# Kernel tuning notes

Measured on AMD Instinct MI355X. Metric: run time of the kernel, lower is better.

Reference implementation:

```python
import jax, jax.numpy as jnp
import numpy as np

B, ES, D, A, E, H, V, T = 8, 14, 2048, 700, 700, 700, 30000, 31


def setup_inputs() -> dict:
    key = jax.random.key(0)
    ks = jax.random.split(key, 16)
    def rn(k, shape, s=0.02):
        return jax.random.normal(k, shape, jnp.float32) * s
    return {
        "encoder_out": jax.random.normal(ks[0], (B, ES, ES, D), jnp.float32),
        "encoded_captions": jax.random.randint(ks[1], (B, T), 0, V),
        "emb": jax.random.uniform(ks[2], (V, E), jnp.float32, -0.1, 0.1),
        "W_enc_att": rn(ks[3], (D, A)), "b_enc_att": jnp.zeros((A,), jnp.float32),
        "W_dec_att": rn(ks[4], (H, A)), "b_dec_att": jnp.zeros((A,), jnp.float32),
        "W_full": rn(ks[5], (A, 1)), "b_full": jnp.zeros((1,), jnp.float32),
        "W_ih": rn(ks[6], (E + D, 4 * H)), "b_ih": jnp.zeros((4 * H,), jnp.float32),
        "W_hh": rn(ks[7], (H, 4 * H)), "b_hh": jnp.zeros((4 * H,), jnp.float32),
        "W_init_h": rn(ks[8], (D, H)), "b_init_h": jnp.zeros((H,), jnp.float32),
        "W_init_c": rn(ks[9], (D, H)), "b_init_c": jnp.zeros((H,), jnp.float32),
        "W_fbeta": rn(ks[10], (H, D)), "b_fbeta": jnp.zeros((D,), jnp.float32),
        "W_fc": jax.random.uniform(ks[11], (H, V), jnp.float32, -0.1, 0.1),
        "b_fc": jnp.zeros((V,), jnp.float32),
    }


def reference(encoder_out, encoded_captions, emb,
              W_enc_att, b_enc_att, W_dec_att, b_dec_att, W_full, b_full,
              W_ih, b_ih, W_hh, b_hh, W_init_h, b_init_h, W_init_c, b_init_c,
              W_fbeta, b_fbeta, W_fc, b_fc):
    # teacher=False path: greedy decode with argmax feedback. Dropout in eval mode (identity).
    Bn = encoder_out.shape[0]
    Dd = encoder_out.shape[-1]
    enc = encoder_out.reshape(Bn, -1, Dd)          # (B, P, D)
    decode_length = encoded_captions.shape[1] - 1
    mean_enc = enc.mean(axis=1)
    h0 = mean_enc @ W_init_h + b_init_h            # (B, H)
    c0 = mean_enc @ W_init_c + b_init_c
    att1 = enc @ W_enc_att + b_enc_att             # (B, P, A) — hoisted out of the loop (same math)
    prev0 = jnp.ones((Bn,), jnp.int32)             # preds initialized to ones

    def step(carry, _):
        h, c, prev = carry
        x_emb = emb[prev]                                          # (B, E)
        att2 = h @ W_dec_att + b_dec_att                           # (B, A)
        e = (jax.nn.relu(att1 + att2[:, None, :]) @ W_full)[..., 0] + b_full[0]  # (B, P)
        alpha = jax.nn.softmax(e, axis=1)
        awe = jnp.einsum('bp,bpd->bd', alpha, enc)                 # attention-weighted encoding
        gate = jax.nn.sigmoid(h @ W_fbeta + b_fbeta)
        awe = gate * awe
        x = jnp.concatenate([x_emb, awe], axis=1)                  # (B, E+D)
        gates = x @ W_ih + b_ih + h @ W_hh + b_hh                  # (B, 4H), torch gate order i,f,g,o
        i, f, g, o = jnp.split(gates, 4, axis=1)
        c_new = jax.nn.sigmoid(f) * c + jax.nn.sigmoid(i) * jnp.tanh(g)
        h_new = jax.nn.sigmoid(o) * jnp.tanh(c_new)
        logits = h_new @ W_fc + b_fc                               # (B, V)
        prev_new = jnp.argmax(logits, axis=1).astype(jnp.int32)
        return (h_new, c_new, prev_new), (logits, alpha)

    _, (logits_seq, alpha_seq) = jax.lax.scan(step, (h0, c0, prev0), None, length=decode_length)
    predictions = jnp.transpose(logits_seq, (1, 0, 2))             # (B, T-1, V)
    alphas = jnp.transpose(alpha_seq, (1, 0, 2))                   # (B, T-1, P)
    return predictions, alphas
```

## Files before the change

### kernel.cpp

```cpp
#include <hip/hip_runtime.h>
#include <math.h>

#define BQ 8
#define PP 196
#define DD 2048
#define AA 700
#define HH 700
#define EE 700
#define VV 30000
#define NSTEP 30
#define G4 2800
#define NA 2748
#define KD 3448

#define KSA 32
#define KRA 22
#define NCBA 11

#define KSD 32
#define KRD 108
#define NCBD 11

#define KSE 6
#define KRE 117
#define NCBE 118
#define NB2 235

__device__ __forceinline__ float sigm(float x) { return 1.f / (1.f + expf(-x)); }

__global__ __launch_bounds__(256) void k_mean(const float* __restrict__ enc,
                                              float* __restrict__ mean) {
    int b = blockIdx.x >> 3;
    int d = ((blockIdx.x & 7) << 8) + threadIdx.x;
    const float* p = enc + (size_t)b * PP * DD + d;
    float s = 0.f;
    for (int i = 0; i < PP; i++) s += p[(size_t)i * DD];
    mean[b * DD + d] = s * (1.0f / PP);
}

__global__ __launch_bounds__(256) void k_init_hc(const float* __restrict__ mean,
    const float* __restrict__ Wh, const float* __restrict__ bh,
    const float* __restrict__ Wc, const float* __restrict__ bc,
    float* __restrict__ h, float* __restrict__ c) {
    __shared__ float X[BQ][DD];
    __shared__ float red[4][64][BQ];
    int tid = threadIdx.x;
    for (int i = tid; i < BQ * DD; i += 256) X[i / DD][i % DD] = mean[i];
    __syncthreads();
    int j = blockIdx.x * 64 + (tid & 63);
    int kq = tid >> 6;
    float acc[BQ];
    #pragma unroll
    for (int b = 0; b < BQ; b++) acc[b] = 0.f;
    if (j < 2 * HH) {
        bool isH = j < HH;
        int col = isH ? j : j - HH;
        const float* wp = (isH ? Wh : Wc) + (size_t)(kq * 512) * HH + col;
        for (int k = kq * 512; k < kq * 512 + 512; k++) {
            float wv = *wp; wp += HH;
            #pragma unroll
            for (int b = 0; b < BQ; b++) acc[b] += X[b][k] * wv;
        }
    }
    #pragma unroll
    for (int b = 0; b < BQ; b++) red[kq][tid & 63][b] = acc[b];
    __syncthreads();
    for (int idx = tid; idx < 512; idx += 256) {
        int jj = idx >> 3, b = idx & 7;
        int jg = blockIdx.x * 64 + jj;
        if (jg >= 2 * HH) continue;
        float s = red[0][jj][b] + red[1][jj][b] + red[2][jj][b] + red[3][jj][b];
        bool isH = jg < HH;
        int col = isH ? jg : jg - HH;
        s += isH ? bh[col] : bc[col];
        (isH ? h : c)[b * HH + col] = s;
    }
}

__global__ __launch_bounds__(256) void k_att1(const float* __restrict__ Aenc,
    const float* __restrict__ W, float* __restrict__ out0,
    float* __restrict__ out1) {
    const int M = BQ * PP;
    __shared__ float As[16][68];
    __shared__ float Bs[16][68];
    int bm = blockIdx.x, bn = blockIdx.y, bz = blockIdx.z;
    int tid = threadIdx.x;
    int tx = tid & 15, ty = tid >> 4;
    float acc[4][4] = {};
    int kbeg = bz * 1024, kend = kbeg + 1024;
    for (int kt = kbeg; kt < kend; kt += 16) {
        {
            int row = tid >> 2, k4 = (tid & 3) * 4;
            int grow = bm * 64 + row;
            float4 v = make_float4(0.f, 0.f, 0.f, 0.f);
            if (grow < M) v = *(const float4*)&Aenc[(size_t)grow * DD + kt + k4];
            As[k4 + 0][row] = v.x; As[k4 + 1][row] = v.y;
            As[k4 + 2][row] = v.z; As[k4 + 3][row] = v.w;
        }
        {
            int rk = tid >> 4, n4 = (tid & 15) * 4;
            int col = bn * 64 + n4;
            float4 wv = make_float4(0.f, 0.f, 0.f, 0.f);
            if (col < AA) wv = *(const float4*)&W[(size_t)(kt + rk) * AA + col];
            *(float4*)&Bs[rk][n4] = wv;
        }
        __syncthreads();
        #pragma unroll
        for (int k = 0; k < 16; k++) {
            float4 a  = *(const float4*)&As[k][ty * 4];
            float4 bv = *(const float4*)&Bs[k][tx * 4];
            float av[4] = {a.x, a.y, a.z, a.w};
            float bb[4] = {bv.x, bv.y, bv.z, bv.w};
            #pragma unroll
            for (int i = 0; i < 4; i++)
                #pragma unroll
                for (int j = 0; j < 4; j++) acc[i][j] += av[i] * bb[j];
        }
        __syncthreads();
    }
    float* out = bz ? out1 : out0;
    for (int i = 0; i < 4; i++) {
        int row = bm * 64 + ty * 4 + i;
        if (row >= M) continue;
        for (int j = 0; j < 4; j++) {
            int col = bn * 64 + tx * 4 + j;
            if (col < AA) out[(size_t)row * AA + col] = acc[i][j];
        }
    }
}

__global__ __launch_bounds__(256) void k_att1red(float* __restrict__ att1,
    const float* __restrict__ part, const float* __restrict__ bias) {
    size_t row = blockIdx.x;
    for (int c = threadIdx.x; c < AA; c += 256)
        att1[row * AA + c] += part[row * AA + c] + bias[c];
}

__global__ __launch_bounds__(256) void k_stepA(const float* __restrict__ h,
    const float* __restrict__ Wda, const float* __restrict__ Wfb,
    float* __restrict__ pA,
    const float* __restrict__ argval, const int* __restrict__ argidx,
    int* __restrict__ prev, int t) {
    int tid = threadIdx.x;
    if (blockIdx.x == NCBA * KSA) {
        int b = tid >> 5, l = tid & 31;
        if (b < 8) {
            if (t == 0) {
                if (l == 0) prev[b] = 1;
            } else {
                float bv = -3.4e38f; int bi = 0x7fffffff;
                for (int vb = l; vb < NB2; vb += 32) {
                    float v = argval[vb * 8 + b]; int ix = argidx[vb * 8 + b];
                    if (v > bv || (v == bv && ix < bi)) { bv = v; bi = ix; }
                }
                #pragma unroll
                for (int off = 16; off; off >>= 1) {
                    float ov = __shfl_down(bv, off, 32);
                    int   oi = __shfl_down(bi, off, 32);
                    if (ov > bv || (ov == bv && oi < bi)) { bv = ov; bi = oi; }
                }
                if (l == 0) prev[b] = bi;
            }
        }
        return;
    }
    __shared__ float s_X[KRA * 8];
    __shared__ float s_red[4 * 64 * 33];
    int cb = blockIdx.x % NCBA, kc = blockIdx.x / NCBA;
    int k0 = kc * KRA;
    int kr = min(KRA, AA - k0);
    for (int i = tid; i < kr * 8; i += 256) {
        int k = i >> 3, b = i & 7;
        s_X[k * 8 + b] = h[b * HH + k0 + k];
    }
    __syncthreads();
    int lane = tid & 63, w = tid >> 6;
    int ka = (w * kr) >> 2, kb = ((w + 1) * kr) >> 2;
    int c0 = cb * 256 + lane * 4;
    float acc[8][4] = {};
    if (c0 < NA) {
        const float* W; int col, ld;
        if (c0 < AA) { W = Wda; col = c0;      ld = AA; }
        else         { W = Wfb; col = c0 - AA; ld = DD; }
        const float* wp = W + (size_t)(k0 + ka) * ld + col;
        #pragma unroll 2
        for (int k = ka; k < kb; ++k) {
            float4 wv = *(const float4*)wp; wp += ld;
            float4 xa = *(const float4*)&s_X[k * 8];
            float4 xb = *(const float4*)&s_X[k * 8 + 4];
            float xv[8] = {xa.x, xa.y, xa.z, xa.w, xb.x, xb.y, xb.z, xb.w};
            #pragma unroll
            for (int b = 0; b < 8; b++) {
                acc[b][0] += xv[b] * wv.x; acc[b][1] += xv[b] * wv.y;
                acc[b][2] += xv[b] * wv.z; acc[b][3] += xv[b] * wv.w;
            }
        }
    }
    float* rr = &s_red[(w * 64 + lane) * 33];
    #pragma unroll
    for (int b = 0; b < 8; b++)
        #pragma unroll
        for (int cc = 0; cc < 4; cc++) rr[cc * 8 + b] = acc[b][cc];
    __syncthreads();
    for (int idx = tid; idx < 2048; idx += 256) {
        int b = idx >> 8, cl = idx & 255;
        int gc = cb * 256 + cl;
        if (gc < NA) {
            int ln = cl >> 2, cc = cl & 3;
            float s = s_red[(0 * 64 + ln) * 33 + cc * 8 + b]
                    + s_red[(1 * 64 + ln) * 33 + cc * 8 + b]
                    + s_red[(2 * 64 + ln) * 33 + cc * 8 + b]
                    + s_red[(3 * 64 + ln) * 33 + cc * 8 + b];
            pA[((size_t)kc * 8 + b) * NA + gc] = s;
        }
    }
}

__global__ __launch_bounds__(256) void k_stepB(const float* __restrict__ pA,
    const float* __restrict__ bda, const float* __restrict__ att1,
    const float* __restrict__ Wf, float* __restrict__ ebuf) {
    int b  = blockIdx.x / 49;
    int p0 = (blockIdx.x % 49) * 4;
    __shared__ float a2[AA];
    __shared__ float wf[AA];
    int tid = threadIdx.x, lane = tid & 63, w = tid >> 6;
    for (int i = tid; i < AA; i += 256) {
        float s = bda[i];
        #pragma unroll 8
        for (int kc = 0; kc < KSA; kc++) s += pA[((size_t)kc * 8 + b) * NA + i];
        a2[i] = s;
        wf[i] = Wf[i];
    }
    __syncthreads();
    int p = p0 + w;
    const float* ap = att1 + (size_t)(b * PP + p) * AA;
    float s = 0.f;
    for (int f4 = lane; f4 < 175; f4 += 64) {
        float4 av = *(const float4*)(ap + f4 * 4);
        float4 tv = *(const float4*)&a2[f4 * 4];
        float4 wv = *(const float4*)&wf[f4 * 4];
        s += fmaxf(av.x + tv.x, 0.f) * wv.x + fmaxf(av.y + tv.y, 0.f) * wv.y
           + fmaxf(av.z + tv.z, 0.f) * wv.z + fmaxf(av.w + tv.w, 0.f) * wv.w;
    }
    #pragma unroll
    for (int off = 32; off; off >>= 1) s += __shfl_down(s, off, 64);
    if (lane == 0) ebuf[b * PP + p] = s;
}

__global__ __launch_bounds__(256) void k_stepC(const float* __restrict__ enc,
    const float* __restrict__ pA, const float* __restrict__ bfb,
    const float* __restrict__ ebuf, float* __restrict__ awe,
    float* __restrict__ oalpha, int t) {
    int b = blockIdx.x >> 3, dc = blockIdx.x & 7;
    __shared__ float s_al[PP];
    __shared__ float s_gate[256];
    __shared__ float s_red[4][256];
    __shared__ float s_rb[8];
    int tid = threadIdx.x, lane = tid & 63, w = tid >> 6;
    float v = (tid < PP) ? ebuf[b * PP + tid] : -3.4e38f;
    float m = v;
    #pragma unroll
    for (int off = 32; off; off >>= 1) m = fmaxf(m, __shfl_down(m, off, 64));
    if (lane == 0) s_rb[w] = m;
    __syncthreads();
    m = fmaxf(fmaxf(s_rb[0], s_rb[1]), fmaxf(s_rb[2], s_rb[3]));
    float ex = (tid < PP) ? expf(v - m) : 0.f;
    float s2 = ex;
    #pragma unroll
    for (int off = 32; off; off >>= 1) s2 += __shfl_down(s2, off, 64);
    if (lane == 0) s_rb[4 + w] = s2;
    __syncthreads();
    float den = s_rb[4] + s_rb[5] + s_rb[6] + s_rb[7];
    if (tid < PP) {
        float al = ex / den;
        s_al[tid] = al;
        if (dc == 0) oalpha[((size_t)b * NSTEP + t) * PP + tid] = al;
    }
    {
        int d = dc * 256 + tid;
        float g = bfb[d];
        #pragma unroll 8
        for (int kc = 0; kc < KSA; kc++) g += pA[((size_t)kc * 8 + b) * NA + AA + d];
        s_gate[tid] = sigm(g);
    }
    __syncthreads();
    int d4 = dc * 256 + lane * 4;
    const float* ep = enc + ((size_t)b * PP + w * 49) * DD + d4;
    float4 acc = make_float4(0.f, 0.f, 0.f, 0.f);
    #pragma unroll 7
    for (int p = 0; p < 49; ++p) {
        float a = s_al[w * 49 + p];
        float4 ev = *(const float4*)ep; ep += DD;
        acc.x += a * ev.x; acc.y += a * ev.y;
        acc.z += a * ev.z; acc.w += a * ev.w;
    }
    *(float4*)&s_red[w][lane * 4] = acc;
    __syncthreads();
    float tot = s_red[0][tid] + s_red[1][tid] + s_red[2][tid] + s_red[3][tid];
    awe[b * DD + dc * 256 + tid] = s_gate[tid] * tot;
}

__global__ __launch_bounds__(256) void k_stepD1(const float* __restrict__ emb,
    const float* __restrict__ awe, const float* __restrict__ h,
    const float* __restrict__ Wih, const float* __restrict__ Whh,
    const int* __restrict__ prev, float* __restrict__ pD) {
    __shared__ float s_X[KRD * 8];
    __shared__ float s_red[4 * 64 * 33];
    __shared__ int s_prev[8];
    int tid = threadIdx.x;
    int cb = blockIdx.x % NCBD, kc = blockIdx.x / NCBD;
    int k0 = kc * KRD;
    int kr = min(KRD, KD - k0);
    if (tid < 8) s_prev[tid] = prev[tid];
    __syncthreads();
    for (int i = tid; i < kr * 8; i += 256) {
        int k = i >> 3, b = i & 7;
        int kg = k0 + k;
        float x;
        if (kg < EE)            x = emb[(size_t)s_prev[b] * EE + kg];
        else if (kg < EE + DD)  x = awe[b * DD + (kg - EE)];
        else                    x = h[b * HH + (kg - EE - DD)];
        s_X[k * 8 + b] = x;
    }
    __syncthreads();
    int lane = tid & 63, w = tid >> 6;
    int ka = (w * kr) >> 2, kb2 = ((w + 1) * kr) >> 2;
    int c0 = cb * 256 + lane * 4;
    float acc[8][4] = {};
    if (c0 < G4) {
        #pragma unroll 2
        for (int k = ka; k < kb2; ++k) {
            int kg = k0 + k;
            const float* wp = (kg < EE + DD)
                ? (Wih + (size_t)kg * G4 + c0)
                : (Whh + (size_t)(kg - EE - DD) * G4 + c0);
            float4 wv = *(const float4*)wp;
            float4 xa = *(const float4*)&s_X[k * 8];
            float4 xb = *(const float4*)&s_X[k * 8 + 4];
            float xv[8] = {xa.x, xa.y, xa.z, xa.w, xb.x, xb.y, xb.z, xb.w};
            #pragma unroll
            for (int b = 0; b < 8; b++) {
                acc[b][0] += xv[b] * wv.x; acc[b][1] += xv[b] * wv.y;
                acc[b][2] += xv[b] * wv.z; acc[b][3] += xv[b] * wv.w;
            }
        }
    }
    float* rr = &s_red[(w * 64 + lane) * 33];
    #pragma unroll
    for (int b = 0; b < 8; b++)
        #pragma unroll
        for (int cc = 0; cc < 4; cc++) rr[cc * 8 + b] = acc[b][cc];
    __syncthreads();
    for (int idx = tid; idx < 2048; idx += 256) {
        int b = idx >> 8, cl = idx & 255;
        int gc = cb * 256 + cl;
        if (gc < G4) {
            int ln = cl >> 2, cc = cl & 3;
            float s = s_red[(0 * 64 + ln) * 33 + cc * 8 + b]
                    + s_red[(1 * 64 + ln) * 33 + cc * 8 + b]
                    + s_red[(2 * 64 + ln) * 33 + cc * 8 + b]
                    + s_red[(3 * 64 + ln) * 33 + cc * 8 + b];
            pD[((size_t)kc * 8 + b) * G4 + gc] = s;
        }
    }
}

__global__ __launch_bounds__(256) void k_stepD2(const float* __restrict__ pD,
    const float* __restrict__ bih, const float* __restrict__ bhh,
    float* __restrict__ c, float* __restrict__ h) {
    __shared__ float sd[4][64][4];
    int tid = threadIdx.x;
    int p = tid & 63, kcg = tid >> 6;
    int oid = blockIdx.x * 64 + p;
    float g0 = 0.f, g1 = 0.f, g2 = 0.f, g3 = 0.f;
    if (oid < BQ * HH) {
        int b = oid / HH, j = oid % HH;
        #pragma unroll
        for (int u = 0; u < 8; ++u) {
            const float* base = pD + ((size_t)(kcg * 8 + u) * 8 + b) * G4;
            g0 += base[j];          g1 += base[HH + j];
            g2 += base[2 * HH + j]; g3 += base[3 * HH + j];
        }
    }
    sd[kcg][p][0] = g0; sd[kcg][p][1] = g1;
    sd[kcg][p][2] = g2; sd[kcg][p][3] = g3;
    __syncthreads();
    if (tid < 64) {
        int oid2 = blockIdx.x * 64 + tid;
        if (oid2 < BQ * HH) {
            int b = oid2 / HH, j = oid2 % HH;
            float s0 = sd[0][tid][0] + sd[1][tid][0] + sd[2][tid][0] + sd[3][tid][0]
                     + bih[j] + bhh[j];
            float s1 = sd[0][tid][1] + sd[1][tid][1] + sd[2][tid][1] + sd[3][tid][1]
                     + bih[HH + j] + bhh[HH + j];
            float s2 = sd[0][tid][2] + sd[1][tid][2] + sd[2][tid][2] + sd[3][tid][2]
                     + bih[2 * HH + j] + bhh[2 * HH + j];
            float s3 = sd[0][tid][3] + sd[1][tid][3] + sd[2][tid][3] + sd[3][tid][3]
                     + bih[3 * HH + j] + bhh[3 * HH + j];
            float ig = sigm(s0), fg = sigm(s1), gg = tanhf(s2), og = sigm(s3);
            float cn = fg * c[b * HH + j] + ig * gg;
            c[b * HH + j] = cn;
            h[b * HH + j] = og * tanhf(cn);
        }
    }
}

__global__ __launch_bounds__(256) void k_stepE1(const float* __restrict__ h,
    const float* __restrict__ Wfc, float* __restrict__ pE) {
    __shared__ float s_X[KRE * 8];
    __shared__ float s_red[4 * 64 * 33];
    int tid = threadIdx.x;
    int cb = blockIdx.x % NCBE, kc = blockIdx.x / NCBE;
    int k0 = kc * KRE;
    int kr = min(KRE, AA - k0);
    for (int i = tid; i < kr * 8; i += 256) {
        int k = i >> 3, b = i & 7;
        s_X[k * 8 + b] = h[b * HH + k0 + k];
    }
    __syncthreads();
    int lane = tid & 63, w = tid >> 6;
    int ka = (w * kr) >> 2, kb = ((w + 1) * kr) >> 2;
    int c0 = cb * 256 + lane * 4;
    float acc[8][4] = {};
    if (c0 < VV) {
        const float* wp = Wfc + (size_t)(k0 + ka) * VV + c0;
        #pragma unroll 2
        for (int k = ka; k < kb; ++k) {
            float4 wv = *(const float4*)wp; wp += VV;
            float4 xa = *(const float4*)&s_X[k * 8];
            float4 xb = *(const float4*)&s_X[k * 8 + 4];
            float xv[8] = {xa.x, xa.y, xa.z, xa.w, xb.x, xb.y, xb.z, xb.w};
            #pragma unroll
            for (int b = 0; b < 8; b++) {
                acc[b][0] += xv[b] * wv.x; acc[b][1] += xv[b] * wv.y;
                acc[b][2] += xv[b] * wv.z; acc[b][3] += xv[b] * wv.w;
            }
        }
    }
    float* rr = &s_red[(w * 64 + lane) * 33];
    #pragma unroll
    for (int b = 0; b < 8; b++)
        #pragma unroll
        for (int cc = 0; cc < 4; cc++) rr[cc * 8 + b] = acc[b][cc];
    __syncthreads();
    for (int idx = tid; idx < 2048; idx += 256) {
        int b = idx >> 8, cl = idx & 255;
        int gc = cb * 256 + cl;
        if (gc < VV) {
            int ln = cl >> 2, cc = cl & 3;
            float s = s_red[(0 * 64 + ln) * 33 + cc * 8 + b]
                    + s_red[(1 * 64 + ln) * 33 + cc * 8 + b]
                    + s_red[(2 * 64 + ln) * 33 + cc * 8 + b]
                    + s_red[(3 * 64 + ln) * 33 + cc * 8 + b];
            pE[((size_t)kc * 8 + b) * VV + gc] = s;
        }
    }
}

__global__ __launch_bounds__(256) void k_stepE2(const float* __restrict__ pE,
    const float* __restrict__ bfc, float* __restrict__ preds,
    float* __restrict__ argval, int* __restrict__ argidx, int t) {
    __shared__ float lg[128][8];
    int tid = threadIdx.x;
    int base = blockIdx.x * 128;
    for (int idx = tid; idx < 1024; idx += 256) {
        int b = idx >> 7, cl = idx & 127;
        int col = base + cl;
        float s = -3.4e38f;
        if (col < VV) {
            s = bfc[col];
            #pragma unroll
            for (int kc = 0; kc < KSE; kc++)
                s += pE[((size_t)kc * 8 + b) * VV + col];
            preds[((size_t)b * NSTEP + t) * VV + col] = s;
        }
        lg[cl][b] = s;
    }
    __syncthreads();
    int b = tid >> 5, l = tid & 31;
    float bv = -3.4e38f; int bi = 0x7fffffff;
    for (int cl = l; cl < 128; cl += 32) {
        float v = lg[cl][b];
        int gi = base + cl;
        if (v > bv || (v == bv && gi < bi)) { bv = v; bi = gi; }
    }
    #pragma unroll
    for (int off = 16; off; off >>= 1) {
        float ov = __shfl_down(bv, off, 32);
        int   oi = __shfl_down(bi, off, 32);
        if (ov > bv || (ov == bv && oi < bi)) { bv = ov; bi = oi; }
    }
    if (l == 0) { argval[blockIdx.x * 8 + b] = bv; argidx[blockIdx.x * 8 + b] = bi; }
}

extern "C" void kernel_launch(void* const* d_in, const int* in_sizes, int n_in,
                              void* d_out, int out_size, void* d_ws, size_t ws_size,
                              hipStream_t stream) {
    (void)in_sizes; (void)n_in; (void)out_size; (void)ws_size;
    const float* enc   = (const float*)d_in[0];
    const float* emb   = (const float*)d_in[2];
    const float* Wea   = (const float*)d_in[3];
    const float* bea   = (const float*)d_in[4];
    const float* Wda   = (const float*)d_in[5];
    const float* bda   = (const float*)d_in[6];
    const float* Wfull = (const float*)d_in[7];
    const float* Wih   = (const float*)d_in[9];
    const float* bih   = (const float*)d_in[10];
    const float* Whh   = (const float*)d_in[11];
    const float* bhh   = (const float*)d_in[12];
    const float* Winh  = (const float*)d_in[13];
    const float* binh  = (const float*)d_in[14];
    const float* Winc  = (const float*)d_in[15];
    const float* binc  = (const float*)d_in[16];
    const float* Wfb   = (const float*)d_in[17];
    const float* bfb   = (const float*)d_in[18];
    const float* Wfc   = (const float*)d_in[19];
    const float* bfc   = (const float*)d_in[20];

    float* preds  = (float*)d_out;
    float* oalpha = preds + (size_t)BQ * NSTEP * VV;

    float* ws = (float*)d_ws;
    float* att1   = ws; ws += (size_t)BQ * PP * AA;
    float* pA     = ws; ws += (size_t)KSA * 8 * NA;
    float* pDE    = ws; ws += (size_t)KSE * 8 * VV;
    float* mean   = ws; ws += BQ * DD;
    float* hbuf   = ws; ws += BQ * HH;
    float* cbuf   = ws; ws += BQ * HH;
    float* ebuf   = ws; ws += BQ * PP;
    float* awe    = ws; ws += BQ * DD;
    float* argval = ws; ws += NB2 * 8;
    int*   argidx = (int*)ws; ws += NB2 * 8;
    int*   prev   = (int*)ws; ws += 16;

    k_mean<<<64, 256, 0, stream>>>(enc, mean);
    k_init_hc<<<22, 256, 0, stream>>>(mean, Winh, binh, Winc, binc, hbuf, cbuf);
    k_att1<<<dim3(25, 11, 2), 256, 0, stream>>>(enc, Wea, att1, pDE);
    k_att1red<<<BQ * PP, 256, 0, stream>>>(att1, pDE, bea);

    for (int t = 0; t < NSTEP; t++) {
        k_stepA<<<NCBA * KSA + 1, 256, 0, stream>>>(hbuf, Wda, Wfb, pA,
                                                    argval, argidx, prev, t);
        k_stepB<<<392, 256, 0, stream>>>(pA, bda, att1, Wfull, ebuf);
        k_stepC<<<64, 256, 0, stream>>>(enc, pA, bfb, ebuf, awe, oalpha, t);
        k_stepD1<<<NCBD * KSD, 256, 0, stream>>>(emb, awe, hbuf, Wih, Whh, prev, pDE);
        k_stepD2<<<88, 256, 0, stream>>>(pDE, bih, bhh, cbuf, hbuf);
        k_stepE1<<<NCBE * KSE, 256, 0, stream>>>(hbuf, Wfc, pDE);
        k_stepE2<<<NB2, 256, 0, stream>>>(pDE, bfc, preds, argval, argidx, t);
    }
}
```

Baseline: 1.866 ms.

## Fuse per-step kernels, use atomic argmax keys, and enlarge att1 GEMM tile

Each step's attention projection (stepA) is merged into the logits GEMM launch of the previous step, with one extra launch before the loop for step 0. The attention score and context kernels (stepB/stepC) become a single kernel. The separate argmax reduction pass is replaced by packed 64-bit atomicMax keys that encode value and index, decoded in stepD1. The att1 GEMM also uses 128-row tiles. Together these cut launches per step from seven to five and remove intermediate buffers. The cost is that the fused BC kernel runs only 64 blocks, each computing all 196 attention scores serially, which may lower parallelism.

```diff
diff --git a/kernel.cpp b/kernel.cpp
--- a/kernel.cpp
+++ b/kernel.cpp
@@ -29,7 +29,9 @@
 __device__ __forceinline__ float sigm(float x) { return 1.f / (1.f + expf(-x)); }
 
 __global__ __launch_bounds__(256) void k_mean(const float* __restrict__ enc,
-                                              float* __restrict__ mean) {
+                                              float* __restrict__ mean,
+                                              unsigned long long* __restrict__ g_arg) {
+    if (blockIdx.x == 0 && threadIdx.x < NSTEP * 8) g_arg[threadIdx.x] = 0ULL;
     int b = blockIdx.x >> 3;
     int d = ((blockIdx.x & 7) << 8) + threadIdx.x;
     const float* p = enc + (size_t)b * PP * DD + d;
@@ -81,17 +83,19 @@
     const float* __restrict__ W, float* __restrict__ out0,
     float* __restrict__ out1) {
     const int M = BQ * PP;
-    __shared__ float As[16][68];
+    __shared__ float As[16][136];
     __shared__ float Bs[16][68];
     int bm = blockIdx.x, bn = blockIdx.y, bz = blockIdx.z;
     int tid = threadIdx.x;
-    int tx = tid & 15, ty = tid >> 4;
-    float acc[4][4] = {};
+    int tr = tid >> 4, tc = tid & 15;
+    float acc[8][4] = {};
     int kbeg = bz * 1024, kend = kbeg + 1024;
     for (int kt = kbeg; kt < kend; kt += 16) {
-        {
-            int row = tid >> 2, k4 = (tid & 3) * 4;
-            int grow = bm * 64 + row;
+        #pragma unroll
+        for (int q = 0; q < 2; ++q) {
+            int f4id = tid + q * 256;
+            int row = f4id >> 2, k4 = (f4id & 3) * 4;
+            int grow = bm * 128 + row;
             float4 v = make_float4(0.f, 0.f, 0.f, 0.f);
             if (grow < M) v = *(const float4*)&Aenc[(size_t)grow * DD + kt + k4];
             As[k4 + 0][row] = v.x; As[k4 + 1][row] = v.y;
@@ -106,24 +110,25 @@
         }
         __syncthreads();
         #pragma unroll
-        for (int k = 0; k < 16; k++) {
-            float4 a  = *(const float4*)&As[k][ty * 4];
-            float4 bv = *(const float4*)&Bs[k][tx * 4];
-            float av[4] = {a.x, a.y, a.z, a.w};
+        for (int k = 0; k < 16; ++k) {
+            float4 a0 = *(const float4*)&As[k][tr * 8];
+            float4 a1 = *(const float4*)&As[k][tr * 8 + 4];
+            float4 bv = *(const float4*)&Bs[k][tc * 4];
+            float av[8] = {a0.x, a0.y, a0.z, a0.w, a1.x, a1.y, a1.z, a1.w};
             float bb[4] = {bv.x, bv.y, bv.z, bv.w};
             #pragma unroll
-            for (int i = 0; i < 4; i++)
+            for (int i = 0; i < 8; i++)
                 #pragma unroll
                 for (int j = 0; j < 4; j++) acc[i][j] += av[i] * bb[j];
         }
         __syncthreads();
     }
     float* out = bz ? out1 : out0;
-    for (int i = 0; i < 4; i++) {
-        int row = bm * 64 + ty * 4 + i;
+    for (int i = 0; i < 8; i++) {
+        int row = bm * 128 + tr * 8 + i;
         if (row >= M) continue;
         for (int j = 0; j < 4; j++) {
-            int col = bn * 64 + tx * 4 + j;
+            int col = bn * 64 + tc * 4 + j;
             if (col < AA) out[(size_t)row * AA + col] = acc[i][j];
         }
     }
@@ -136,128 +141,52 @@
         att1[row * AA + c] += part[row * AA + c] + bias[c];
 }
 
-__global__ __launch_bounds__(256) void k_stepA(const float* __restrict__ h,
-    const float* __restrict__ Wda, const float* __restrict__ Wfb,
-    float* __restrict__ pA,
-    const float* __restrict__ argval, const int* __restrict__ argidx,
-    int* __restrict__ prev, int t) {
-    int tid = threadIdx.x;
-    if (blockIdx.x == NCBA * KSA) {
-        int b = tid >> 5, l = tid & 31;
-        if (b < 8) {
-            if (t == 0) {
-                if (l == 0) prev[b] = 1;
-            } else {
-                float bv = -3.4e38f; int bi = 0x7fffffff;
-                for (int vb = l; vb < NB2; vb += 32) {
-                    float v = argval[vb * 8 + b]; int ix = argidx[vb * 8 + b];
-                    if (v > bv || (v == bv && ix < bi)) { bv = v; bi = ix; }
-                }
-                #pragma unroll
-                for (int off = 16; off; off >>= 1) {
-                    float ov = __shfl_down(bv, off, 32);
-                    int   oi = __shfl_down(bi, off, 32);
-                    if (ov > bv || (ov == bv && oi < bi)) { bv = ov; bi = oi; }
-                }
-                if (l == 0) prev[b] = bi;
-            }
-        }
-        return;
-    }
-    __shared__ float s_X[KRA * 8];
-    __shared__ float s_red[4 * 64 * 33];
-    int cb = blockIdx.x % NCBA, kc = blockIdx.x / NCBA;
-    int k0 = kc * KRA;
-    int kr = min(KRA, AA - k0);
-    for (int i = tid; i < kr * 8; i += 256) {
-        int k = i >> 3, b = i & 7;
-        s_X[k * 8 + b] = h[b * HH + k0 + k];
-    }
-    __syncthreads();
-    int lane = tid & 63, w = tid >> 6;
-    int ka = (w * kr) >> 2, kb = ((w + 1) * kr) >> 2;
-    int c0 = cb * 256 + lane * 4;
-    float acc[8][4] = {};
-    if (c0 < NA) {
-        const float* W; int col, ld;
-        if (c0 < AA) { W = Wda; col = c0;      ld = AA; }
-        else         { W = Wfb; col = c0 - AA; ld = DD; }
-        const float* wp = W + (size_t)(k0 + ka) * ld + col;
-        #pragma unroll 2
-        for (int k = ka; k < kb; ++k) {
-            float4 wv = *(const float4*)wp; wp += ld;
-            float4 xa = *(const float4*)&s_X[k * 8];
-            float4 xb = *(const float4*)&s_X[k * 8 + 4];
-            float xv[8] = {xa.x, xa.y, xa.z, xa.w, xb.x, xb.y, xb.z, xb.w};
-            #pragma unroll
-            for (int b = 0; b < 8; b++) {
-                acc[b][0] += xv[b] * wv.x; acc[b][1] += xv[b] * wv.y;
-                acc[b][2] += xv[b] * wv.z; acc[b][3] += xv[b] * wv.w;
-            }
-        }
-    }
-    float* rr = &s_red[(w * 64 + lane) * 33];
-    #pragma unroll
-    for (int b = 0; b < 8; b++)
-        #pragma unroll
-        for (int cc = 0; cc < 4; cc++) rr[cc * 8 + b] = acc[b][cc];
-    __syncthreads();
-    for (int idx = tid; idx < 2048; idx += 256) {
-        int b = idx >> 8, cl = idx & 255;
-        int gc = cb * 256 + cl;
-        if (gc < NA) {
-            int ln = cl >> 2, cc = cl & 3;
-            float s = s_red[(0 * 64 + ln) * 33 + cc * 8 + b]
-                    + s_red[(1 * 64 + ln) * 33 + cc * 8 + b]
-                    + s_red[(2 * 64 + ln) * 33 + cc * 8 + b]
-                    + s_red[(3 * 64 + ln) * 33 + cc * 8 + b];
-            pA[((size_t)kc * 8 + b) * NA + gc] = s;
-        }
-    }
-}
-
-__global__ __launch_bounds__(256) void k_stepB(const float* __restrict__ pA,
-    const float* __restrict__ bda, const float* __restrict__ att1,
-    const float* __restrict__ Wf, float* __restrict__ ebuf) {
-    int b  = blockIdx.x / 49;
-    int p0 = (blockIdx.x % 49) * 4;
-    __shared__ float a2[AA];
-    __shared__ float wf[AA];
+__global__ __launch_bounds__(256) void k_stepBC(const float* __restrict__ enc,
+    const float* __restrict__ pA, const float* __restrict__ bda,
+    const float* __restrict__ bfb, const float* __restrict__ att1,
+    const float* __restrict__ Wf, float* __restrict__ awe,
+    float* __restrict__ oalpha, int t) {
+    int b = blockIdx.x >> 3, dc = blockIdx.x & 7;
+    __shared__ float s_a2[AA];
+    __shared__ float s_wf[AA];
+    __shared__ float s_gate[256];
+    __shared__ float s_e[PP];
+    __shared__ float s_al[PP];
+    __shared__ float s_red[4][256];
+    __shared__ float s_rb[8];
     int tid = threadIdx.x, lane = tid & 63, w = tid >> 6;
     for (int i = tid; i < AA; i += 256) {
         float s = bda[i];
         #pragma unroll 8
         for (int kc = 0; kc < KSA; kc++) s += pA[((size_t)kc * 8 + b) * NA + i];
-        a2[i] = s;
-        wf[i] = Wf[i];
-    }
-    __syncthreads();
-    int p = p0 + w;
-    const float* ap = att1 + (size_t)(b * PP + p) * AA;
-    float s = 0.f;
-    for (int f4 = lane; f4 < 175; f4 += 64) {
-        float4 av = *(const float4*)(ap + f4 * 4);
-        float4 tv = *(const float4*)&a2[f4 * 4];
-        float4 wv = *(const float4*)&wf[f4 * 4];
-        s += fmaxf(av.x + tv.x, 0.f) * wv.x + fmaxf(av.y + tv.y, 0.f) * wv.y
-           + fmaxf(av.z + tv.z, 0.f) * wv.z + fmaxf(av.w + tv.w, 0.f) * wv.w;
-    }
-    #pragma unroll
-    for (int off = 32; off; off >>= 1) s += __shfl_down(s, off, 64);
-    if (lane == 0) ebuf[b * PP + p] = s;
-}
-
-__global__ __launch_bounds__(256) void k_stepC(const float* __restrict__ enc,
-    const float* __restrict__ pA, const float* __restrict__ bfb,
-    const float* __restrict__ ebuf, float* __restrict__ awe,
-    float* __restrict__ oalpha, int t) {
-    int b = blockIdx.x >> 3, dc = blockIdx.x & 7;
-    __shared__ float s_al[PP];
-    __shared__ float s_gate[256];
-    __shared__ float s_red[4][256];
-    __shared__ float s_rb[8];
-    int tid = threadIdx.x, lane = tid & 63, w = tid >> 6;
-    float v = (tid < PP) ? ebuf[b * PP + tid] : -3.4e38f;
+        s_a2[i] = s;
+        s_wf[i] = Wf[i];
+    }
+    {
+        int d = dc * 256 + tid;
+        float g = bfb[d];
+        #pragma unroll 8
+        for (int kc = 0; kc < KSA; kc++) g += pA[((size_t)kc * 8 + b) * NA + AA + d];
+        s_gate[tid] = sigm(g);
+    }
+    __syncthreads();
+    for (int i = 0; i < 49; ++i) {
+        int p = w * 49 + i;
+        const float* ap = att1 + (size_t)(b * PP + p) * AA;
+        float s = 0.f;
+        for (int f4 = lane; f4 < 175; f4 += 64) {
+            float4 av = *(const float4*)(ap + f4 * 4);
+            float4 tv = *(const float4*)&s_a2[f4 * 4];
+            float4 wv = *(const float4*)&s_wf[f4 * 4];
+            s += fmaxf(av.x + tv.x, 0.f) * wv.x + fmaxf(av.y + tv.y, 0.f) * wv.y
+               + fmaxf(av.z + tv.z, 0.f) * wv.z + fmaxf(av.w + tv.w, 0.f) * wv.w;
+        }
+        #pragma unroll
+        for (int off = 32; off; off >>= 1) s += __shfl_down(s, off, 64);
+        if (lane == 0) s_e[p] = s;
+    }
+    __syncthreads();
+    float v = (tid < PP) ? s_e[tid] : -3.4e38f;
     float m = v;
     #pragma unroll
     for (int off = 32; off; off >>= 1) m = fmaxf(m, __shfl_down(m, off, 64));
@@ -276,25 +205,18 @@
         s_al[tid] = al;
         if (dc == 0) oalpha[((size_t)b * NSTEP + t) * PP + tid] = al;
     }
-    {
-        int d = dc * 256 + tid;
-        float g = bfb[d];
-        #pragma unroll 8
-        for (int kc = 0; kc < KSA; kc++) g += pA[((size_t)kc * 8 + b) * NA + AA + d];
-        s_gate[tid] = sigm(g);
-    }
     __syncthreads();
     int d4 = dc * 256 + lane * 4;
     const float* ep = enc + ((size_t)b * PP + w * 49) * DD + d4;
-    float4 acc = make_float4(0.f, 0.f, 0.f, 0.f);
+    float4 accv = make_float4(0.f, 0.f, 0.f, 0.f);
     #pragma unroll 7
     for (int p = 0; p < 49; ++p) {
         float a = s_al[w * 49 + p];
         float4 ev = *(const float4*)ep; ep += DD;
-        acc.x += a * ev.x; acc.y += a * ev.y;
-        acc.z += a * ev.z; acc.w += a * ev.w;
-    }
-    *(float4*)&s_red[w][lane * 4] = acc;
+        accv.x += a * ev.x; accv.y += a * ev.y;
+        accv.z += a * ev.z; accv.w += a * ev.w;
+    }
+    *(float4*)&s_red[w][lane * 4] = accv;
     __syncthreads();
     float tot = s_red[0][tid] + s_red[1][tid] + s_red[2][tid] + s_red[3][tid];
     awe[b * DD + dc * 256 + tid] = s_gate[tid] * tot;
@@ -303,7 +225,7 @@
 __global__ __launch_bounds__(256) void k_stepD1(const float* __restrict__ emb,
     const float* __restrict__ awe, const float* __restrict__ h,
     const float* __restrict__ Wih, const float* __restrict__ Whh,
-    const int* __restrict__ prev, float* __restrict__ pD) {
+    const unsigned long long* __restrict__ g_arg, float* __restrict__ pD, int t) {
     __shared__ float s_X[KRD * 8];
     __shared__ float s_red[4 * 64 * 33];
     __shared__ int s_prev[8];
@@ -311,7 +233,13 @@
     int cb = blockIdx.x % NCBD, kc = blockIdx.x / NCBD;
     int k0 = kc * KRD;
     int kr = min(KRD, KD - k0);
-    if (tid < 8) s_prev[tid] = prev[tid];
+    if (tid < 8) {
+        if (t == 0) s_prev[tid] = 1;
+        else {
+            unsigned long long key = g_arg[(t - 1) * 8 + tid];
+            s_prev[tid] = (int)(0xFFFFFFFFu - (unsigned)(key & 0xFFFFFFFFull));
+        }
+    }
     __syncthreads();
     for (int i = tid; i < kr * 8; i += 256) {
         int k = i >> 3, b = i & 7;
@@ -405,61 +333,119 @@
     }
 }
 
-__global__ __launch_bounds__(256) void k_stepE1(const float* __restrict__ h,
-    const float* __restrict__ Wfc, float* __restrict__ pE) {
+__global__ __launch_bounds__(256) void k_stepEA(const float* __restrict__ h,
+    const float* __restrict__ Wfc, float* __restrict__ pE,
+    const float* __restrict__ Wda, const float* __restrict__ Wfb,
+    float* __restrict__ pA, int only_a) {
     __shared__ float s_X[KRE * 8];
     __shared__ float s_red[4 * 64 * 33];
     int tid = threadIdx.x;
-    int cb = blockIdx.x % NCBE, kc = blockIdx.x / NCBE;
-    int k0 = kc * KRE;
-    int kr = min(KRE, AA - k0);
-    for (int i = tid; i < kr * 8; i += 256) {
-        int k = i >> 3, b = i & 7;
-        s_X[k * 8 + b] = h[b * HH + k0 + k];
-    }
-    __syncthreads();
+    int bx = blockIdx.x;
     int lane = tid & 63, w = tid >> 6;
-    int ka = (w * kr) >> 2, kb = ((w + 1) * kr) >> 2;
-    int c0 = cb * 256 + lane * 4;
-    float acc[8][4] = {};
-    if (c0 < VV) {
-        const float* wp = Wfc + (size_t)(k0 + ka) * VV + c0;
-        #pragma unroll 2
-        for (int k = ka; k < kb; ++k) {
-            float4 wv = *(const float4*)wp; wp += VV;
-            float4 xa = *(const float4*)&s_X[k * 8];
-            float4 xb = *(const float4*)&s_X[k * 8 + 4];
-            float xv[8] = {xa.x, xa.y, xa.z, xa.w, xb.x, xb.y, xb.z, xb.w};
+    bool doA; int abid = 0;
+    if (only_a)                { doA = true;  abid = bx; }
+    else if (bx >= NCBE * KSE) { doA = true;  abid = bx - NCBE * KSE; }
+    else                       { doA = false; }
+
+    if (doA) {
+        int cb = abid % NCBA, kc = abid / NCBA;
+        int k0 = kc * KRA;
+        int kr = min(KRA, AA - k0);
+        for (int i = tid; i < kr * 8; i += 256) {
+            int k = i >> 3, b = i & 7;
+            s_X[k * 8 + b] = h[b * HH + k0 + k];
+        }
+        __syncthreads();
+        int ka = (w * kr) >> 2, kb = ((w + 1) * kr) >> 2;
+        int c0 = cb * 256 + lane * 4;
+        float acc[8][4] = {};
+        if (c0 < NA) {
+            const float* W; int col, ld;
+            if (c0 < AA) { W = Wda; col = c0;      ld = AA; }
+            else         { W = Wfb; col = c0 - AA; ld = DD; }
+            const float* wp = W + (size_t)(k0 + ka) * ld + col;
+            #pragma unroll 2
+            for (int k = ka; k < kb; ++k) {
+                float4 wv = *(const float4*)wp; wp += ld;
+                float4 xa = *(const float4*)&s_X[k * 8];
+                float4 xb = *(const float4*)&s_X[k * 8 + 4];
+                float xv[8] = {xa.x, xa.y, xa.z, xa.w, xb.x, xb.y, xb.z, xb.w};
+                #pragma unroll
+                for (int b = 0; b < 8; b++) {
+                    acc[b][0] += xv[b] * wv.x; acc[b][1] += xv[b] * wv.y;
+                    acc[b][2] += xv[b] * wv.z; acc[b][3] += xv[b] * wv.w;
+                }
+            }
+        }
+        float* rr = &s_red[(w * 64 + lane) * 33];
+        #pragma unroll
+        for (int b = 0; b < 8; b++)
             #pragma unroll
-            for (int b = 0; b < 8; b++) {
-                acc[b][0] += xv[b] * wv.x; acc[b][1] += xv[b] * wv.y;
-                acc[b][2] += xv[b] * wv.z; acc[b][3] += xv[b] * wv.w;
+            for (int cc = 0; cc < 4; cc++) rr[cc * 8 + b] = acc[b][cc];
+        __syncthreads();
+        for (int idx = tid; idx < 2048; idx += 256) {
+            int b = idx >> 8, cl = idx & 255;
+            int gc = cb * 256 + cl;
+            if (gc < NA) {
+                int ln = cl >> 2, cc = cl & 3;
+                float s = s_red[(0 * 64 + ln) * 33 + cc * 8 + b]
+                        + s_red[(1 * 64 + ln) * 33 + cc * 8 + b]
+                        + s_red[(2 * 64 + ln) * 33 + cc * 8 + b]
+                        + s_red[(3 * 64 + ln) * 33 + cc * 8 + b];
+                pA[((size_t)kc * 8 + b) * NA + gc] = s;
             }
         }
-    }
-    float* rr = &s_red[(w * 64 + lane) * 33];
-    #pragma unroll
-    for (int b = 0; b < 8; b++)
-        #pragma unroll
-        for (int cc = 0; cc < 4; cc++) rr[cc * 8 + b] = acc[b][cc];
-    __syncthreads();
-    for (int idx = tid; idx < 2048; idx += 256) {
-        int b = idx >> 8, cl = idx & 255;
-        int gc = cb * 256 + cl;
-        if (gc < VV) {
-            int ln = cl >> 2, cc = cl & 3;
-            float s = s_red[(0 * 64 + ln) * 33 + cc * 8 + b]
-                    + s_red[(1 * 64 + ln) * 33 + cc * 8 + b]
-                    + s_red[(2 * 64 + ln) * 33 + cc * 8 + b]
-                    + s_red[(3 * 64 + ln) * 33 + cc * 8 + b];
-            pE[((size_t)kc * 8 + b) * VV + gc] = s;
+    } else {
+        int cb = bx % NCBE, kc = bx / NCBE;
+        int k0 = kc * KRE;
+        int kr = min(KRE, AA - k0);
+        for (int i = tid; i < kr * 8; i += 256) {
+            int k = i >> 3, b = i & 7;
+            s_X[k * 8 + b] = h[b * HH + k0 + k];
+        }
+        __syncthreads();
+        int ka = (w * kr) >> 2, kb = ((w + 1) * kr) >> 2;
+        int c0 = cb * 256 + lane * 4;
+        float acc[8][4] = {};
+        if (c0 < VV) {
+            const float* wp = Wfc + (size_t)(k0 + ka) * VV + c0;
+            #pragma unroll 2
+            for (int k = ka; k < kb; ++k) {
+                float4 wv = *(const float4*)wp; wp += VV;
+                float4 xa = *(const float4*)&s_X[k * 8];
+                float4 xb = *(const float4*)&s_X[k * 8 + 4];
+                float xv[8] = {xa.x, xa.y, xa.z, xa.w, xb.x, xb.y, xb.z, xb.w};
+                #pragma unroll
+                for (int b = 0; b < 8; b++) {
+                    acc[b][0] += xv[b] * wv.x; acc[b][1] += xv[b] * wv.y;
+                    acc[b][2] += xv[b] * wv.z; acc[b][3] += xv[b] * wv.w;
+                }
+            }
+        }
+        float* rr = &s_red[(w * 64 + lane) * 33];
+        #pragma unroll
+        for (int b = 0; b < 8; b++)
+            #pragma unroll
+            for (int cc = 0; cc < 4; cc++) rr[cc * 8 + b] = acc[b][cc];
+        __syncthreads();
+        for (int idx = tid; idx < 2048; idx += 256) {
+            int b = idx >> 8, cl = idx & 255;
+            int gc = cb * 256 + cl;
+            if (gc < VV) {
+                int ln = cl >> 2, cc = cl & 3;
+                float s = s_red[(0 * 64 + ln) * 33 + cc * 8 + b]
+                        + s_red[(1 * 64 + ln) * 33 + cc * 8 + b]
+                        + s_red[(2 * 64 + ln) * 33 + cc * 8 + b]
+                        + s_red[(3 * 64 + ln) * 33 + cc * 8 + b];
+                pE[((size_t)kc * 8 + b) * VV + gc] = s;
+            }
         }
     }
 }
 
 __global__ __launch_bounds__(256) void k_stepE2(const float* __restrict__ pE,
     const float* __restrict__ bfc, float* __restrict__ preds,
-    float* __restrict__ argval, int* __restrict__ argidx, int t) {
+    unsigned long long* __restrict__ g_arg, int t) {
     __shared__ float lg[128][8];
     int tid = threadIdx.x;
     int base = blockIdx.x * 128;
@@ -490,7 +476,13 @@
         int   oi = __shfl_down(bi, off, 32);
         if (ov > bv || (ov == bv && oi < bi)) { bv = ov; bi = oi; }
     }
-    if (l == 0) { argval[blockIdx.x * 8 + b] = bv; argidx[blockIdx.x * 8 + b] = bi; }
+    if (l == 0 && bi < VV) {
+        unsigned fb = __float_as_uint(bv);
+        fb = (fb & 0x80000000u) ? ~fb : (fb | 0x80000000u);
+        unsigned long long key = ((unsigned long long)fb << 32)
+                               | (unsigned long long)(0xFFFFFFFFu - (unsigned)bi);
+        atomicMax(&g_arg[t * 8 + b], key);
+    }
 }
 
 extern "C" void kernel_launch(void* const* d_in, const int* in_sizes, int n_in,
@@ -520,32 +512,30 @@
     float* preds  = (float*)d_out;
     float* oalpha = preds + (size_t)BQ * NSTEP * VV;
 
-    float* ws = (float*)d_ws;
-    float* att1   = ws; ws += (size_t)BQ * PP * AA;
-    float* pA     = ws; ws += (size_t)KSA * 8 * NA;
-    float* pDE    = ws; ws += (size_t)KSE * 8 * VV;
-    float* mean   = ws; ws += BQ * DD;
-    float* hbuf   = ws; ws += BQ * HH;
-    float* cbuf   = ws; ws += BQ * HH;
-    float* ebuf   = ws; ws += BQ * PP;
-    float* awe    = ws; ws += BQ * DD;
-    float* argval = ws; ws += NB2 * 8;
-    int*   argidx = (int*)ws; ws += NB2 * 8;
-    int*   prev   = (int*)ws; ws += 16;
-
-    k_mean<<<64, 256, 0, stream>>>(enc, mean);
+    unsigned long long* g_arg = (unsigned long long*)d_ws;
+    float* ws = (float*)d_ws + 480;
+    float* att1 = ws; ws += (size_t)BQ * PP * AA;
+    float* pA   = ws; ws += (size_t)KSA * 8 * NA;
+    float* pDE  = ws; ws += (size_t)KSE * 8 * VV;
+    float* mean = ws; ws += BQ * DD;
+    float* hbuf = ws; ws += BQ * HH;
+    float* cbuf = ws; ws += BQ * HH;
+    float* awe  = ws; ws += BQ * DD;
+
+    k_mean<<<64, 256, 0, stream>>>(enc, mean, g_arg);
     k_init_hc<<<22, 256, 0, stream>>>(mean, Winh, binh, Winc, binc, hbuf, cbuf);
-    k_att1<<<dim3(25, 11, 2), 256, 0, stream>>>(enc, Wea, att1, pDE);
+    k_att1<<<dim3(13, 11, 2), 256, 0, stream>>>(enc, Wea, att1, pDE);
     k_att1red<<<BQ * PP, 256, 0, stream>>>(att1, pDE, bea);
+    k_stepEA<<<NCBA * KSA, 256, 0, stream>>>(hbuf, Wfc, pDE, Wda, Wfb, pA, 1);
 
     for (int t = 0; t < NSTEP; t++) {
-        k_stepA<<<NCBA * KSA + 1, 256, 0, stream>>>(hbuf, Wda, Wfb, pA,
-                                                    argval, argidx, prev, t);
-        k_stepB<<<392, 256, 0, stream>>>(pA, bda, att1, Wfull, ebuf);
-        k_stepC<<<64, 256, 0, stream>>>(enc, pA, bfb, ebuf, awe, oalpha, t);
-        k_stepD1<<<NCBD * KSD, 256, 0, stream>>>(emb, awe, hbuf, Wih, Whh, prev, pDE);
+        k_stepBC<<<64, 256, 0, stream>>>(enc, pA, bda, bfb, att1, Wfull,
+                                         awe, oalpha, t);
+        k_stepD1<<<NCBD * KSD, 256, 0, stream>>>(emb, awe, hbuf, Wih, Whh,
+                                                 g_arg, pDE, t);
         k_stepD2<<<88, 256, 0, stream>>>(pDE, bih, bhh, cbuf, hbuf);
-        k_stepE1<<<NCBE * KSE, 256, 0, stream>>>(hbuf, Wfc, pDE);
-        k_stepE2<<<NB2, 256, 0, stream>>>(pDE, bfc, preds, argval, argidx, t);
-    }
-}
+        k_stepEA<<<NCBE * KSE + NCBA * KSA, 256, 0, stream>>>(hbuf, Wfc, pDE,
+                                                              Wda, Wfb, pA, 0);
+        k_stepE2<<<NB2, 256, 0, stream>>>(pDE, bfc, preds, g_arg, t);
+    }
+}
```

After: 3.674 ms. +96.9%, slower.
